# Optimization experiments

Hardware: AMD Instinct MI355X
Metric: run time of the kernel (lower is better)

Reference implementation:

```python
import jax, jax.numpy as jnp
import numpy as np

NUM_NODES = 65536       # B * gcn_nodes_num = 256 * 256
NODES_PER_GRAPH = 256
GCN_EMB_DIM = 128
N_EMBD = 512
NUM_EDGES = 1048576     # avg degree 16
NEG_SLOPE = 0.1


def gcn_conv(x, edge_index, W, b, num_nodes):
    """PyG GCNConv: add self-loops, symmetric normalization, linear, aggregate."""
    loop = jnp.arange(num_nodes, dtype=edge_index.dtype)
    src = jnp.concatenate([edge_index[0], loop])
    dst = jnp.concatenate([edge_index[1], loop])
    deg = jax.ops.segment_sum(jnp.ones_like(dst, dtype=x.dtype), dst,
                              num_segments=num_nodes)
    dinv = jnp.where(deg > 0, jax.lax.rsqrt(deg), jnp.zeros_like(deg))
    norm = dinv[src] * dinv[dst]              # [E+N]
    h = x @ W                                 # [N, out]
    msg = h[src] * norm[:, None]              # [E+N, out]
    out = jax.ops.segment_sum(msg, dst, num_segments=num_nodes)
    return out + b


def setup_inputs() -> dict:
    key = jax.random.key(0)
    ks = jax.random.split(key, 8)
    nodes = jax.random.normal(ks[0], (NUM_NODES, 3), dtype=jnp.float32)
    edge_index = jax.random.randint(ks[1], (2, NUM_EDGES), 0, NUM_NODES,
                                    dtype=jnp.int64)
    W1 = jax.random.normal(ks[2], (3, 3), dtype=jnp.float32) * 0.5
    b1 = jnp.zeros((3,), dtype=jnp.float32)
    W2 = jax.random.normal(ks[3], (3, GCN_EMB_DIM), dtype=jnp.float32) * 0.5
    b2 = jnp.zeros((GCN_EMB_DIM,), dtype=jnp.float32)
    W3 = jax.random.normal(ks[4], (GCN_EMB_DIM * NODES_PER_GRAPH, N_EMBD),
                           dtype=jnp.float32) * 0.01
    b3 = jnp.zeros((N_EMBD,), dtype=jnp.float32)
    return {"nodes": nodes, "edge_index": edge_index,
            "W1": W1, "b1": b1, "W2": W2, "b2": b2, "W3": W3, "b3": b3}


def reference(nodes, edge_index, W1, b1, W2, b2, W3, b3):
    n = nodes.shape[0]
    h = gcn_conv(nodes, edge_index, W1, b1, n)           # GCNConv(3,3)
    h = jnp.where(h >= 0, h, NEG_SLOPE * h)              # leaky_relu(0.1)
    h = gcn_conv(h, edge_index, W2, b2, n)               # GCNConv(3,128)
    h = h.reshape(-1, GCN_EMB_DIM * NODES_PER_GRAPH)     # [B, 128*256]
    out = h @ W3 + b3                                    # [B, 512]
    return out
```

## Files before the change

kernel.cpp:

```cpp
#include <hip/hip_runtime.h>

static constexpr int NN   = 65536;
static constexpr int NPG  = 256;
static constexpr int NB   = 256;
static constexpr int EMB  = 128;
static constexpr int NOUT = 512;

static constexpr int NBIN = 256;
static constexpr int CAP  = 4608;

static constexpr int BT = 8;
static constexpr int KS = 16;
static constexpr int IC = NPG / KS;

__global__ __launch_bounds__(1024)
void k_part(const int* __restrict__ src, const int* __restrict__ dst, int E,
            int* __restrict__ gbin, int* __restrict__ part) {
    __shared__ int hist[NBIN], loff[NBIN], base[NBIN], scanbuf[NBIN];
    __shared__ int stage[4096];
    int tid = threadIdx.x;
    int epb = (E + gridDim.x - 1) / gridDim.x;
    int e0 = blockIdx.x * epb;
    int e1 = min(e0 + epb, E);
    if (tid < NBIN) hist[tid] = 0;
    __syncthreads();

    int pk[4], bn[4], rk[4];
    int n = 0;
    for (int e = e0 + tid; e < e1; e += 1024) {
        int s = src[e], d = dst[e];
        pk[n] = s | ((d & 255) << 16);
        bn[n] = d >> 8;
        rk[n] = atomicAdd(&hist[bn[n]], 1);
        n++;
    }
    __syncthreads();

    if (tid < NBIN) scanbuf[tid] = hist[tid];
    __syncthreads();
    for (int off = 1; off < NBIN; off <<= 1) {
        int v = 0;
        if (tid < NBIN && tid >= off) v = scanbuf[tid - off];
        __syncthreads();
        if (tid < NBIN) scanbuf[tid] += v;
        __syncthreads();
    }
    if (tid < NBIN) {
        loff[tid] = scanbuf[tid] - hist[tid];
        base[tid] = atomicAdd(&gbin[tid], hist[tid]);
    }
    __syncthreads();

    for (int k = 0; k < n; k++) stage[loff[bn[k]] + rk[k]] = pk[k];
    __syncthreads();

    int bin = tid >> 2;
    int cnt = hist[bin], bs = base[bin], lo = loff[bin];
    for (int t = tid & 3; t < cnt; t += 4) {
        int gp = bs + t;
        if (gp < CAP) part[bin * CAP + gp] = stage[lo + t];
    }
}

__global__ void k_degprep(const int* __restrict__ gbin, const int* __restrict__ part,
                          const float* __restrict__ nodes,
                          float* __restrict__ dinv, float4* __restrict__ y1) {
    __shared__ int hist[NPG];
    int tid = threadIdx.x, bin = blockIdx.x;
    hist[tid] = 0;
    __syncthreads();
    int cnt = min(gbin[bin], CAP);
    const int* pp = part + (size_t)bin * CAP;
    for (int e = tid; e < cnt; e += 256)
        atomicAdd(&hist[(pp[e] >> 16) & 255], 1);
    __syncthreads();
    int node = bin * NPG + tid;
    float di = rsqrtf((float)(hist[tid] + 1));
    dinv[node] = di;
    y1[node] = make_float4(nodes[3*node+0] * di, nodes[3*node+1] * di,
                           nodes[3*node+2] * di, 0.f);
}

__global__ __launch_bounds__(1024)
void k_agg1(const int* __restrict__ gbin, const int* __restrict__ part,
            const float* __restrict__ dinv, const float4* __restrict__ y1,
            const float* __restrict__ W1, const float* __restrict__ b1,
            float4* __restrict__ y2) {
    __shared__ float accx[NPG], accy[NPG], accz[NPG];
    int tid = threadIdx.x, bin = blockIdx.x;
    if (tid < NPG) { accx[tid] = 0.f; accy[tid] = 0.f; accz[tid] = 0.f; }
    __syncthreads();
    int cnt = min(gbin[bin], CAP);
    const int* pp = part + (size_t)bin * CAP;
    for (int e = tid; e < cnt; e += 1024) {
        int p = pp[e];
        int s = p & 0xFFFF, dlow = (p >> 16) & 255;
        float4 v = y1[s];
        atomicAdd(&accx[dlow], v.x);
        atomicAdd(&accy[dlow], v.y);
        atomicAdd(&accz[dlow], v.z);
    }
    __syncthreads();
    if (tid < NPG) {
        int node = bin * NPG + tid;
        float4 self = y1[node];
        float di = dinv[node];
        float a0 = (accx[tid] + self.x) * di;
        float a1 = (accy[tid] + self.y) * di;
        float a2 = (accz[tid] + self.z) * di;
        float h[3];
#pragma unroll
        for (int k = 0; k < 3; k++) {
            float t = a0 * W1[0*3+k] + a1 * W1[1*3+k] + a2 * W1[2*3+k] + b1[k];
            t = (t >= 0.f) ? t : 0.1f * t;
            h[k] = t * di;
        }
        y2[node] = make_float4(h[0], h[1], h[2], 0.f);
    }
}

__global__ __launch_bounds__(1024)
void k_agg2(const int* __restrict__ gbin, const int* __restrict__ part,
            const float* __restrict__ dinv, const float4* __restrict__ y2,
            float4* __restrict__ agg2) {
    __shared__ float accx[NPG], accy[NPG], accz[NPG];
    int tid = threadIdx.x, bin = blockIdx.x;
    if (tid < NPG) { accx[tid] = 0.f; accy[tid] = 0.f; accz[tid] = 0.f; }
    __syncthreads();
    int cnt = min(gbin[bin], CAP);
    const int* pp = part + (size_t)bin * CAP;
    for (int e = tid; e < cnt; e += 1024) {
        int p = pp[e];
        int s = p & 0xFFFF, dlow = (p >> 16) & 255;
        float4 v = y2[s];
        atomicAdd(&accx[dlow], v.x);
        atomicAdd(&accy[dlow], v.y);
        atomicAdd(&accz[dlow], v.z);
    }
    __syncthreads();
    if (tid < NPG) {
        int node = bin * NPG + tid;
        float4 self = y2[node];
        float di = dinv[node];
        agg2[node] = make_float4((accx[tid] + self.x) * di,
                                 (accy[tid] + self.y) * di,
                                 (accz[tid] + self.z) * di, 0.f);
    }
}

__global__ void k_buildV(const float* __restrict__ W2, const float* __restrict__ b2,
                         const float* __restrict__ W3, float* __restrict__ V) {
    int i = blockIdx.x;
    int j = blockIdx.y * 256 + threadIdx.x;
    float acc0 = 0.f, acc1 = 0.f, acc2 = 0.f, acc3 = 0.f;
    const float* w3 = W3 + (size_t)i * EMB * NOUT + j;
    for (int c = 0; c < EMB; c++) {
        float v = w3[(size_t)c * NOUT];
        acc0 += W2[0*EMB+c] * v;
        acc1 += W2[1*EMB+c] * v;
        acc2 += W2[2*EMB+c] * v;
        acc3 += b2[c]       * v;
    }
    float* o = V + (size_t)i * 4 * NOUT + j;
    o[0*NOUT] = acc0; o[1*NOUT] = acc1; o[2*NOUT] = acc2; o[3*NOUT] = acc3;
}

__global__ void k_out_part(const float4* __restrict__ agg2, const float* __restrict__ V,
                           float* __restrict__ part) {
    __shared__ float4 a_s[BT * IC];
    int tid = threadIdx.x;
    int j  = blockIdx.x * 256 + tid;
    int b0 = blockIdx.y * BT;
    int i0 = blockIdx.z * IC;
    for (int idx = tid; idx < BT * IC; idx += 256) {
        int t = idx / IC, i = idx % IC;
        a_s[idx] = agg2[(size_t)(b0 + t) * NPG + i0 + i];
    }
    __syncthreads();

    float acc[BT];
#pragma unroll
    for (int t = 0; t < BT; t++) acc[t] = 0.f;

    const float* vj = V + (size_t)i0 * 4 * NOUT + j;
    for (int i = 0; i < IC; i++) {
        float v0 = vj[(size_t)(i*4+0) * NOUT];
        float v1 = vj[(size_t)(i*4+1) * NOUT];
        float v2 = vj[(size_t)(i*4+2) * NOUT];
        float v3 = vj[(size_t)(i*4+3) * NOUT];
#pragma unroll
        for (int t = 0; t < BT; t++) {
            float4 a = a_s[t*IC + i];
            acc[t] += a.x * v0 + a.y * v1 + a.z * v2 + v3;
        }
    }
#pragma unroll
    for (int t = 0; t < BT; t++)
        part[((size_t)blockIdx.z * NB + b0 + t) * NOUT + j] = acc[t];
}

__global__ void k_reduce(const float* __restrict__ part, const float* __restrict__ b3,
                         float* __restrict__ out) {
    int idx = blockIdx.x * 256 + threadIdx.x;
    int j = idx & (NOUT - 1);
    float acc = b3[j];
#pragma unroll
    for (int s = 0; s < KS; s++) acc += part[(size_t)s * NB * NOUT + idx];
    out[idx] = acc;
}

extern "C" void kernel_launch(void* const* d_in, const int* in_sizes, int n_in,
                              void* d_out, int out_size, void* d_ws, size_t ws_size,
                              hipStream_t stream) {
    const float* nodes = (const float*)d_in[0];
    const int*   ei    = (const int*)  d_in[1];
    const float* W1    = (const float*)d_in[2];
    const float* b1    = (const float*)d_in[3];
    const float* W2    = (const float*)d_in[4];
    const float* b2    = (const float*)d_in[5];
    const float* W3    = (const float*)d_in[6];
    const float* b3    = (const float*)d_in[7];
    float* out = (float*)d_out;

    const int E = in_sizes[1] / 2;
    const int* src = ei;
    const int* dst = ei + E;

    char* ws = (char*)d_ws;
    int*    gbin  = (int*)ws;
    int*    partE = (int*)(ws + 1024);
    float*  dinv  = (float*)(partE + (size_t)NBIN * CAP);
    float4* y1    = (float4*)(dinv + NN);
    float4* y2    = y1 + NN;
    float4* agg2  = y2 + NN;
    float*  V     = (float*)(agg2 + NN);
    float*  partO = V + (size_t)NPG * 4 * NOUT;

    hipMemsetAsync(gbin, 0, NBIN * 4, stream);
    k_part    <<<NBIN, 1024, 0, stream>>>(src, dst, E, gbin, partE);
    k_degprep <<<NBIN,  256, 0, stream>>>(gbin, partE, nodes, dinv, y1);
    k_agg1    <<<NBIN, 1024, 0, stream>>>(gbin, partE, dinv, y1, W1, b1, y2);
    k_agg2    <<<NBIN, 1024, 0, stream>>>(gbin, partE, dinv, y2, agg2);
    k_buildV  <<<dim3(256, 2),       256, 0, stream>>>(W2, b2, W3, V);
    k_out_part<<<dim3(2, NB/BT, KS), 256, 0, stream>>>(agg2, V, partO);
    k_reduce  <<<NB*NOUT/256,        256, 0, stream>>>(partO, b3, out);
}
```

Before: 186.5 us.

## Build per-bin CSR and gather-based aggregation; fuse V build into partition kernel

Adds a per-bin counting sort in the degree kernel that produces a CSR layout (row start/degree packed ints plus 16-bit source ids), so both aggregation kernels become atomic-free gathers with four lanes per node and shuffle reductions instead of shared-memory float atomics. The W2·W3 precomputation is merged into the partition kernel as extra blocks so it overlaps with edge partitioning, which removes one launch. Partition loads now use int4 vector loads, which assumes each thread covers at most 4 edges per block. The cost is extra sort work and shared memory in the CSR kernel, in exchange for cheaper aggregation passes.

```diff
diff --git a/kernel.cpp b/kernel.cpp
--- a/kernel.cpp
+++ b/kernel.cpp
@@ -8,31 +8,67 @@
 
 static constexpr int NBIN = 256;
 static constexpr int CAP  = 4608;
+static constexpr int VBLK = 128;
 
 static constexpr int BT = 8;
 static constexpr int KS = 16;
 static constexpr int IC = NPG / KS;
 
 __global__ __launch_bounds__(1024)
-void k_part(const int* __restrict__ src, const int* __restrict__ dst, int E,
-            int* __restrict__ gbin, int* __restrict__ part) {
+void k_partV(const int* __restrict__ src, const int* __restrict__ dst, int E,
+             int* __restrict__ gbin, int* __restrict__ part,
+             const float* __restrict__ W2, const float* __restrict__ b2,
+             const float* __restrict__ W3, float* __restrict__ V) {
+    int tid = threadIdx.x;
+    int bid = blockIdx.x;
+    if (bid >= NBIN) {
+        int vb = bid - NBIN;
+        int i = vb * 2 + (tid >> 9);
+        int j = tid & 511;
+        float acc0 = 0.f, acc1 = 0.f, acc2 = 0.f, acc3 = 0.f;
+        const float* w3 = W3 + (size_t)i * EMB * NOUT + j;
+        for (int c = 0; c < EMB; c++) {
+            float v = w3[(size_t)c * NOUT];
+            acc0 += W2[0*EMB+c] * v;
+            acc1 += W2[1*EMB+c] * v;
+            acc2 += W2[2*EMB+c] * v;
+            acc3 += b2[c]       * v;
+        }
+        float* o = V + (size_t)i * 4 * NOUT + j;
+        o[0*NOUT] = acc0; o[1*NOUT] = acc1; o[2*NOUT] = acc2; o[3*NOUT] = acc3;
+        return;
+    }
     __shared__ int hist[NBIN], loff[NBIN], base[NBIN], scanbuf[NBIN];
     __shared__ int stage[4096];
-    int tid = threadIdx.x;
-    int epb = (E + gridDim.x - 1) / gridDim.x;
-    int e0 = blockIdx.x * epb;
+    int epb = (E + NBIN - 1) / NBIN;
+    int e0 = bid * epb;
     int e1 = min(e0 + epb, E);
     if (tid < NBIN) hist[tid] = 0;
     __syncthreads();
 
     int pk[4], bn[4], rk[4];
     int n = 0;
-    for (int e = e0 + tid; e < e1; e += 1024) {
-        int s = src[e], d = dst[e];
-        pk[n] = s | ((d & 255) << 16);
-        bn[n] = d >> 8;
-        rk[n] = atomicAdd(&hist[bn[n]], 1);
-        n++;
+    int e = e0 + tid * 4;
+    if (e + 4 <= e1) {
+        int4 s4 = *(const int4*)(src + e);
+        int4 d4 = *(const int4*)(dst + e);
+        int ss[4] = {s4.x, s4.y, s4.z, s4.w};
+        int dd[4] = {d4.x, d4.y, d4.z, d4.w};
+#pragma unroll
+        for (int k = 0; k < 4; k++) {
+            pk[k] = ss[k] | ((dd[k] & 255) << 16);
+            bn[k] = dd[k] >> 8;
+            rk[k] = atomicAdd(&hist[bn[k]], 1);
+        }
+        n = 4;
+    } else {
+        for (int k = 0; k < 4 && e + k < e1; k++) {
+            int s = src[e+k], d = dst[e+k];
+            pk[n] = s | ((d & 255) << 16);
+            bn[n] = d >> 8;
+            rk[n] = atomicAdd(&hist[bn[n]], 1);
+            n++;
+        }
     }
     __syncthreads();
 
@@ -62,52 +98,72 @@
     }
 }
 
-__global__ void k_degprep(const int* __restrict__ gbin, const int* __restrict__ part,
-                          const float* __restrict__ nodes,
-                          float* __restrict__ dinv, float4* __restrict__ y1) {
-    __shared__ int hist[NPG];
+__global__ void k_csr(const int* __restrict__ gbin, const int* __restrict__ part,
+                      const float* __restrict__ nodes,
+                      float* __restrict__ dinv, float4* __restrict__ y1,
+                      int* __restrict__ rs, unsigned short* __restrict__ srt) {
+    __shared__ int pkst[CAP];
+    __shared__ int hist[NPG], scanb[NPG], off_[NPG];
+    __shared__ unsigned short stageS[CAP];
     int tid = threadIdx.x, bin = blockIdx.x;
     hist[tid] = 0;
     __syncthreads();
     int cnt = min(gbin[bin], CAP);
     const int* pp = part + (size_t)bin * CAP;
-    for (int e = tid; e < cnt; e += 256)
-        atomicAdd(&hist[(pp[e] >> 16) & 255], 1);
-    __syncthreads();
+    for (int e = tid; e < cnt; e += 256) {
+        int p = pp[e];
+        pkst[e] = p;
+        atomicAdd(&hist[(p >> 16) & 255], 1);
+    }
+    __syncthreads();
+    scanb[tid] = hist[tid];
+    __syncthreads();
+    for (int off = 1; off < NPG; off <<= 1) {
+        int v = (tid >= off) ? scanb[tid - off] : 0;
+        __syncthreads();
+        scanb[tid] += v;
+        __syncthreads();
+    }
+    int start = scanb[tid] - hist[tid];
+    off_[tid] = start;
     int node = bin * NPG + tid;
     float di = rsqrtf((float)(hist[tid] + 1));
     dinv[node] = di;
     y1[node] = make_float4(nodes[3*node+0] * di, nodes[3*node+1] * di,
                            nodes[3*node+2] * di, 0.f);
-}
-
-__global__ __launch_bounds__(1024)
-void k_agg1(const int* __restrict__ gbin, const int* __restrict__ part,
-            const float* __restrict__ dinv, const float4* __restrict__ y1,
-            const float* __restrict__ W1, const float* __restrict__ b1,
-            float4* __restrict__ y2) {
-    __shared__ float accx[NPG], accy[NPG], accz[NPG];
-    int tid = threadIdx.x, bin = blockIdx.x;
-    if (tid < NPG) { accx[tid] = 0.f; accy[tid] = 0.f; accz[tid] = 0.f; }
-    __syncthreads();
-    int cnt = min(gbin[bin], CAP);
-    const int* pp = part + (size_t)bin * CAP;
-    for (int e = tid; e < cnt; e += 1024) {
-        int p = pp[e];
-        int s = p & 0xFFFF, dlow = (p >> 16) & 255;
-        float4 v = y1[s];
-        atomicAdd(&accx[dlow], v.x);
-        atomicAdd(&accy[dlow], v.y);
-        atomicAdd(&accz[dlow], v.z);
-    }
-    __syncthreads();
-    if (tid < NPG) {
-        int node = bin * NPG + tid;
-        float4 self = y1[node];
-        float di = dinv[node];
-        float a0 = (accx[tid] + self.x) * di;
-        float a1 = (accy[tid] + self.y) * di;
-        float a2 = (accz[tid] + self.z) * di;
+    rs[node] = start | (hist[tid] << 20);
+    __syncthreads();
+    for (int e = tid; e < cnt; e += 256) {
+        int p = pkst[e];
+        int pos = atomicAdd(&off_[(p >> 16) & 255], 1);
+        stageS[pos] = (unsigned short)(p & 0xFFFF);
+    }
+    __syncthreads();
+    const unsigned int* so = (const unsigned int*)stageS;
+    unsigned int* g = (unsigned int*)(srt + (size_t)bin * CAP);
+    for (int t = tid; t < (cnt + 1) >> 1; t += 256) g[t] = so[t];
+}
+
+__global__ void k_agg1(const int* __restrict__ rs, const unsigned short* __restrict__ srt,
+                       const float* __restrict__ dinv, const float4* __restrict__ y1,
+                       const float* __restrict__ W1, const float* __restrict__ b1,
+                       float4* __restrict__ y2) {
+    int gid = blockIdx.x * 256 + threadIdx.x;
+    int i = gid >> 2, sub = gid & 3;
+    int rsd = rs[i];
+    int start = rsd & 0xFFFFF, deg = rsd >> 20;
+    const unsigned short* sp = srt + (size_t)(i >> 8) * CAP + start;
+    float ax = 0.f, ay = 0.f, az = 0.f;
+    for (int k = sub; k < deg; k += 4) {
+        float4 v = y1[sp[k]];
+        ax += v.x; ay += v.y; az += v.z;
+    }
+    ax += __shfl_xor(ax, 1); ay += __shfl_xor(ay, 1); az += __shfl_xor(az, 1);
+    ax += __shfl_xor(ax, 2); ay += __shfl_xor(ay, 2); az += __shfl_xor(az, 2);
+    if (sub == 0) {
+        float4 self = y1[i];
+        float di = dinv[i];
+        float a0 = (ax + self.x) * di, a1 = (ay + self.y) * di, a2 = (az + self.z) * di;
         float h[3];
 #pragma unroll
         for (int k = 0; k < 3; k++) {
@@ -115,54 +171,31 @@
             t = (t >= 0.f) ? t : 0.1f * t;
             h[k] = t * di;
         }
-        y2[node] = make_float4(h[0], h[1], h[2], 0.f);
-    }
-}
-
-__global__ __launch_bounds__(1024)
-void k_agg2(const int* __restrict__ gbin, const int* __restrict__ part,
-            const float* __restrict__ dinv, const float4* __restrict__ y2,
-            float4* __restrict__ agg2) {
-    __shared__ float accx[NPG], accy[NPG], accz[NPG];
-    int tid = threadIdx.x, bin = blockIdx.x;
-    if (tid < NPG) { accx[tid] = 0.f; accy[tid] = 0.f; accz[tid] = 0.f; }
-    __syncthreads();
-    int cnt = min(gbin[bin], CAP);
-    const int* pp = part + (size_t)bin * CAP;
-    for (int e = tid; e < cnt; e += 1024) {
-        int p = pp[e];
-        int s = p & 0xFFFF, dlow = (p >> 16) & 255;
-        float4 v = y2[s];
-        atomicAdd(&accx[dlow], v.x);
-        atomicAdd(&accy[dlow], v.y);
-        atomicAdd(&accz[dlow], v.z);
-    }
-    __syncthreads();
-    if (tid < NPG) {
-        int node = bin * NPG + tid;
-        float4 self = y2[node];
-        float di = dinv[node];
-        agg2[node] = make_float4((accx[tid] + self.x) * di,
-                                 (accy[tid] + self.y) * di,
-                                 (accz[tid] + self.z) * di, 0.f);
-    }
-}
-
-__global__ void k_buildV(const float* __restrict__ W2, const float* __restrict__ b2,
-                         const float* __restrict__ W3, float* __restrict__ V) {
-    int i = blockIdx.x;
-    int j = blockIdx.y * 256 + threadIdx.x;
-    float acc0 = 0.f, acc1 = 0.f, acc2 = 0.f, acc3 = 0.f;
-    const float* w3 = W3 + (size_t)i * EMB * NOUT + j;
-    for (int c = 0; c < EMB; c++) {
-        float v = w3[(size_t)c * NOUT];
-        acc0 += W2[0*EMB+c] * v;
-        acc1 += W2[1*EMB+c] * v;
-        acc2 += W2[2*EMB+c] * v;
-        acc3 += b2[c]       * v;
-    }
-    float* o = V + (size_t)i * 4 * NOUT + j;
-    o[0*NOUT] = acc0; o[1*NOUT] = acc1; o[2*NOUT] = acc2; o[3*NOUT] = acc3;
+        y2[i] = make_float4(h[0], h[1], h[2], 0.f);
+    }
+}
+
+__global__ void k_agg2(const int* __restrict__ rs, const unsigned short* __restrict__ srt,
+                       const float* __restrict__ dinv, const float4* __restrict__ y2,
+                       float4* __restrict__ agg2) {
+    int gid = blockIdx.x * 256 + threadIdx.x;
+    int i = gid >> 2, sub = gid & 3;
+    int rsd = rs[i];
+    int start = rsd & 0xFFFFF, deg = rsd >> 20;
+    const unsigned short* sp = srt + (size_t)(i >> 8) * CAP + start;
+    float ax = 0.f, ay = 0.f, az = 0.f;
+    for (int k = sub; k < deg; k += 4) {
+        float4 v = y2[sp[k]];
+        ax += v.x; ay += v.y; az += v.z;
+    }
+    ax += __shfl_xor(ax, 1); ay += __shfl_xor(ay, 1); az += __shfl_xor(az, 1);
+    ax += __shfl_xor(ax, 2); ay += __shfl_xor(ay, 2); az += __shfl_xor(az, 2);
+    if (sub == 0) {
+        float4 self = y2[i];
+        float di = dinv[i];
+        agg2[i] = make_float4((ax + self.x) * di, (ay + self.y) * di,
+                              (az + self.z) * di, 0.f);
+    }
 }
 
 __global__ void k_out_part(const float4* __restrict__ agg2, const float* __restrict__ V,
@@ -227,21 +260,22 @@
     const int* dst = ei + E;
 
     char* ws = (char*)d_ws;
-    int*    gbin  = (int*)ws;
-    int*    partE = (int*)(ws + 1024);
-    float*  dinv  = (float*)(partE + (size_t)NBIN * CAP);
-    float4* y1    = (float4*)(dinv + NN);
+    float4* y1    = (float4*)ws;
     float4* y2    = y1 + NN;
     float4* agg2  = y2 + NN;
     float*  V     = (float*)(agg2 + NN);
     float*  partO = V + (size_t)NPG * 4 * NOUT;
+    int*    partE = (int*)(partO + (size_t)KS * NB * NOUT);
+    unsigned short* srt = (unsigned short*)(partE + (size_t)NBIN * CAP);
+    int*    rs    = (int*)(srt + (size_t)NBIN * CAP);
+    float*  dinv  = (float*)(rs + NN);
+    int*    gbin  = (int*)(dinv + NN);
 
     hipMemsetAsync(gbin, 0, NBIN * 4, stream);
-    k_part    <<<NBIN, 1024, 0, stream>>>(src, dst, E, gbin, partE);
-    k_degprep <<<NBIN,  256, 0, stream>>>(gbin, partE, nodes, dinv, y1);
-    k_agg1    <<<NBIN, 1024, 0, stream>>>(gbin, partE, dinv, y1, W1, b1, y2);
-    k_agg2    <<<NBIN, 1024, 0, stream>>>(gbin, partE, dinv, y2, agg2);
-    k_buildV  <<<dim3(256, 2),       256, 0, stream>>>(W2, b2, W3, V);
+    k_partV   <<<NBIN + VBLK, 1024, 0, stream>>>(src, dst, E, gbin, partE, W2, b2, W3, V);
+    k_csr     <<<NBIN,  256, 0, stream>>>(gbin, partE, nodes, dinv, y1, rs, srt);
+    k_agg1    <<<NN*4/256, 256, 0, stream>>>(rs, srt, dinv, y1, W1, b1, y2);
+    k_agg2    <<<NN*4/256, 256, 0, stream>>>(rs, srt, dinv, y2, agg2);
     k_out_part<<<dim3(2, NB/BT, KS), 256, 0, stream>>>(agg2, V, partO);
     k_reduce  <<<NB*NOUT/256,        256, 0, stream>>>(partO, b3, out);
 }
```

Measured after the change: 166.8 us. -10.6%, faster.
